# Performance work log

Hardware: AMD Instinct MI355X
Metric: run time of the kernel (lower is better)

Reference implementation:

```python
import jax, jax.numpy as jnp
import numpy as np

F = 128  # num_features
N = 200000

def setup_inputs() -> dict:
    key = jax.random.key(0)
    ks = jax.random.split(key, 9)
    s = 0.05
    inp = {
        "node_feat": jax.random.normal(ks[0], (N, 4 * F), dtype=jnp.float32),
        "U_w": jax.random.normal(ks[1], (F, F), dtype=jnp.float32) * s,
        "U_b": jax.random.normal(ks[2], (F,), dtype=jnp.float32) * s,
        "V_w": jax.random.normal(ks[3], (F, F), dtype=jnp.float32) * s,
        "V_b": jax.random.normal(ks[4], (F,), dtype=jnp.float32) * s,
        "m1_w": jax.random.normal(ks[5], (2 * F, F), dtype=jnp.float32) * s,
        "m1_b": jax.random.normal(ks[6], (F,), dtype=jnp.float32) * s,
        "m2_w": jax.random.normal(ks[7], (F, 3 * F), dtype=jnp.float32) * s,
        "m2_b": jax.random.normal(ks[8], (3 * F,), dtype=jnp.float32) * s,
    }
    return inp

def reference(node_feat, U_w, U_b, V_w, V_b, m1_w, m1_b, m2_w, m2_b):
    node_scalar = node_feat[:, :F]                       # [N, F]
    node_vector = node_feat[:, F:].reshape(-1, 3, F)     # [N, 3, F]
    Uv = jnp.einsum('ncf,fg->ncg', node_vector, U_w) + U_b  # [N, 3, F]
    Vv = jnp.einsum('ncf,fg->ncg', node_vector, V_w) + V_b  # [N, 3, F]
    Vv_norm = jnp.linalg.norm(Vv, axis=1)                # [N, F]
    mlp_in = jnp.concatenate((Vv_norm, node_scalar), axis=1)  # [N, 2F]
    h = jax.nn.silu(mlp_in @ m1_w + m1_b)                # [N, F]
    mlp_out = h @ m2_w + m2_b                            # [N, 3F]
    a_vv, a_sv, a_ss = jnp.split(mlp_out, 3, axis=1)
    delta_v = a_vv[:, None, :] * Uv                      # [N, 3, F]
    inner_prod = jnp.sum(Uv * Vv, axis=1)                # [N, F]
    delta_s = a_sv * inner_prod + a_ss                   # [N, F]
    residual = jnp.concatenate([delta_s, delta_v.reshape(-1, 3 * F)], axis=1)
    return node_feat + residual
```

## Files before the change

kernel.cpp:

```cpp
#include <hip/hip_runtime.h>


#define NT 32
#define STRA 136
#define STRM 264
#define STRH 136

typedef __attribute__((ext_vector_type(8))) short bf16x8;
typedef __attribute__((ext_vector_type(4))) short short4v;
typedef __attribute__((ext_vector_type(4))) float f32x4;

#define MFMA16(a, b, c) __builtin_amdgcn_mfma_f32_16x16x32_bf16(a, b, c, 0, 0, 0)

__device__ __forceinline__ short f2bf(float x) {
    union { float f; unsigned u; } v; v.f = x;
    unsigned r = v.u + 0x7fffu + ((v.u >> 16) & 1u);
    return (short)(r >> 16);
}

__global__ void prep_weights(const float* __restrict__ Uw, const float* __restrict__ Vw,
                             const float* __restrict__ m1w, const float* __restrict__ m2w,
                             short* __restrict__ ws) {
    int idx = blockIdx.x * 256 + threadIdx.x;
    if (idx < 16384) {
        int g = idx >> 7, k = idx & 127;
        ws[idx]         = f2bf(Uw[k * 128 + g]);
        ws[16384 + idx] = f2bf(Vw[k * 128 + g]);
    } else if (idx < 49152) {
        int j = idx - 16384;
        int g = j >> 8, k = j & 255;
        ws[32768 + j] = f2bf(m1w[k * 128 + g]);
    } else if (idx < 98304) {
        int j = idx - 49152;
        int g = j >> 7, k = j & 127;
        ws[65536 + j] = f2bf(m2w[k * 384 + g]);
    }
}

__global__ __launch_bounds__(256, 2)
void painn_fused(const float* __restrict__ nf,
                 const float* __restrict__ Ub, const float* __restrict__ Vb,
                 const float* __restrict__ m1b, const float* __restrict__ m2b,
                 const short* __restrict__ wbuf,
                 float* __restrict__ out) {
    extern __shared__ short lds[];
    short* smA = lds;
    short* smM = smA + 96 * STRA;
    short* smH = smM + 32 * STRM;

    const short* Ut  = wbuf;
    const short* Vt  = wbuf + 16384;
    const short* M1t = wbuf + 32768;
    const short* M2t = wbuf + 65536;

    const int tid  = threadIdx.x;
    const int wave = tid >> 6;
    const int lane = tid & 63;
    const int fc   = lane & 15;
    const int quad = lane >> 4;
    const int ntg0 = wave * 2;
    const long nodebase = (long)blockIdx.x * NT;

    {
        const float* src = nf + nodebase * 512;
        #pragma unroll
        for (int it = 0; it < 16; ++it) {
            int chunk = tid + 256 * it;
            int n = chunk >> 7;
            int col = (chunk & 127) << 2;
            const float4 v = *(const float4*)(src + n * 512 + col);
            short4v s;
            s.x = f2bf(v.x); s.y = f2bf(v.y); s.z = f2bf(v.z); s.w = f2bf(v.w);
            if (col < 128) {
                *(short4v*)&smM[n * STRM + 128 + col] = s;
            } else {
                int vc = col - 128;
                int c = vc >> 7, k = vc & 127;
                *(short4v*)&smA[(c * 32 + n) * STRA + k] = s;
            }
        }
    }
    __syncthreads();

    f32x4 accU[2][3][2], accV[2][3][2];
    #pragma unroll
    for (int nt = 0; nt < 2; ++nt)
        #pragma unroll
        for (int c = 0; c < 3; ++c)
            #pragma unroll
            for (int s = 0; s < 2; ++s) { accU[nt][c][s] = (f32x4)(0.0f); accV[nt][c][s] = (f32x4)(0.0f); }

    #pragma unroll
    for (int kb = 0; kb < 4; ++kb) {
        const int koff = kb * 32 + quad * 8;
        bf16x8 af[3][2];
        #pragma unroll
        for (int c = 0; c < 3; ++c)
            #pragma unroll
            for (int s = 0; s < 2; ++s)
                af[c][s] = *(const bf16x8*)&smA[(c * 32 + s * 16 + fc) * STRA + koff];
        bf16x8 bu[2], bv[2];
        #pragma unroll
        for (int nt = 0; nt < 2; ++nt) {
            const int g = (ntg0 + nt) * 16 + fc;
            bu[nt] = *(const bf16x8*)&Ut[g * 128 + koff];
            bv[nt] = *(const bf16x8*)&Vt[g * 128 + koff];
        }
        #pragma unroll
        for (int nt = 0; nt < 2; ++nt)
            #pragma unroll
            for (int c = 0; c < 3; ++c)
                #pragma unroll
                for (int s = 0; s < 2; ++s) {
                    accU[nt][c][s] = MFMA16(af[c][s], bu[nt], accU[nt][c][s]);
                    accV[nt][c][s] = MFMA16(af[c][s], bv[nt], accV[nt][c][s]);
                }
    }

    float inner[2][2][4];
    #pragma unroll
    for (int nt = 0; nt < 2; ++nt) {
        const int g = (ntg0 + nt) * 16 + fc;
        const float ub = Ub[g], vb = Vb[g];
        #pragma unroll
        for (int s = 0; s < 2; ++s)
            #pragma unroll
            for (int i = 0; i < 4; ++i) {
                float u0 = accU[nt][0][s][i] + ub;
                float u1 = accU[nt][1][s][i] + ub;
                float u2 = accU[nt][2][s][i] + ub;
                float v0 = accV[nt][0][s][i] + vb;
                float v1 = accV[nt][1][s][i] + vb;
                float v2 = accV[nt][2][s][i] + vb;
                accU[nt][0][s][i] = u0; accU[nt][1][s][i] = u1; accU[nt][2][s][i] = u2;
                inner[nt][s][i] = u0 * v0 + u1 * v1 + u2 * v2;
                const float nrm = sqrtf(v0 * v0 + v1 * v1 + v2 * v2);
                const int nl = s * 16 + quad * 4 + i;
                smM[nl * STRM + g] = f2bf(nrm);
            }
    }
    __syncthreads();

    f32x4 acc2[2][2];
    #pragma unroll
    for (int nt = 0; nt < 2; ++nt) { acc2[nt][0] = (f32x4)(0.0f); acc2[nt][1] = (f32x4)(0.0f); }
    #pragma unroll
    for (int kb = 0; kb < 8; ++kb) {
        const int koff = kb * 32 + quad * 8;
        bf16x8 a0 = *(const bf16x8*)&smM[fc * STRM + koff];
        bf16x8 a1 = *(const bf16x8*)&smM[(16 + fc) * STRM + koff];
        #pragma unroll
        for (int nt = 0; nt < 2; ++nt) {
            const int g = (ntg0 + nt) * 16 + fc;
            bf16x8 b = *(const bf16x8*)&M1t[g * 256 + koff];
            acc2[nt][0] = MFMA16(a0, b, acc2[nt][0]);
            acc2[nt][1] = MFMA16(a1, b, acc2[nt][1]);
        }
    }
    #pragma unroll
    for (int nt = 0; nt < 2; ++nt) {
        const int g = (ntg0 + nt) * 16 + fc;
        const float bb = m1b[g];
        #pragma unroll
        for (int mt = 0; mt < 2; ++mt)
            #pragma unroll
            for (int i = 0; i < 4; ++i) {
                const float x = acc2[nt][mt][i] + bb;
                const float sl = x / (1.0f + __expf(-x));
                const int nl = mt * 16 + quad * 4 + i;
                smH[nl * STRH + g] = f2bf(sl);
            }
    }
    __syncthreads();

    f32x4 acc3[3][2][2];
    #pragma unroll
    for (int p = 0; p < 3; ++p)
        #pragma unroll
        for (int nt = 0; nt < 2; ++nt) { acc3[p][nt][0] = (f32x4)(0.0f); acc3[p][nt][1] = (f32x4)(0.0f); }
    #pragma unroll
    for (int kb = 0; kb < 4; ++kb) {
        const int koff = kb * 32 + quad * 8;
        bf16x8 a0 = *(const bf16x8*)&smH[fc * STRH + koff];
        bf16x8 a1 = *(const bf16x8*)&smH[(16 + fc) * STRH + koff];
        #pragma unroll
        for (int p = 0; p < 3; ++p)
            #pragma unroll
            for (int nt = 0; nt < 2; ++nt) {
                const int gcol = p * 128 + (ntg0 + nt) * 16 + fc;
                bf16x8 b = *(const bf16x8*)&M2t[gcol * 128 + koff];
                acc3[p][nt][0] = MFMA16(a0, b, acc3[p][nt][0]);
                acc3[p][nt][1] = MFMA16(a1, b, acc3[p][nt][1]);
            }
    }

    #pragma unroll
    for (int nt = 0; nt < 2; ++nt) {
        const int g = (ntg0 + nt) * 16 + fc;
        const float bvv = m2b[g], bsv = m2b[128 + g], bss = m2b[256 + g];
        #pragma unroll
        for (int mt = 0; mt < 2; ++mt)
            #pragma unroll
            for (int i = 0; i < 4; ++i) {
                const int nl = mt * 16 + quad * 4 + i;
                const long base = (nodebase + nl) * 512;
                const float avv = acc3[0][nt][mt][i] + bvv;
                const float asv = acc3[1][nt][mt][i] + bsv;
                const float ass = acc3[2][nt][mt][i] + bss;
                const float ds  = asv * inner[nt][mt][i] + ass;
                out[base + g] = nf[base + g] + ds;
                #pragma unroll
                for (int c = 0; c < 3; ++c) {
                    const float dv = avv * accU[nt][c][mt][i];
                    out[base + 128 + c * 128 + g] = nf[base + 128 + c * 128 + g] + dv;
                }
            }
    }
}

extern "C" void kernel_launch(void* const* d_in, const int* in_sizes, int n_in,
                              void* d_out, int out_size, void* d_ws, size_t ws_size,
                              hipStream_t stream) {
    (void)in_sizes; (void)n_in; (void)out_size; (void)ws_size;
    const float* node_feat = (const float*)d_in[0];
    const float* U_w  = (const float*)d_in[1];
    const float* U_b  = (const float*)d_in[2];
    const float* V_w  = (const float*)d_in[3];
    const float* V_b  = (const float*)d_in[4];
    const float* m1_w = (const float*)d_in[5];
    const float* m1_b = (const float*)d_in[6];
    const float* m2_w = (const float*)d_in[7];
    const float* m2_b = (const float*)d_in[8];
    short* wbuf = (short*)d_ws;

    prep_weights<<<384, 256, 0, stream>>>(U_w, V_w, m1_w, m2_w, wbuf);

    const int nblocks = 200000 / NT;
    const size_t lds_bytes = (size_t)(96 * STRA + 32 * STRM + 32 * STRH) * sizeof(short);
    painn_fused<<<nblocks, 256, lds_bytes, stream>>>(
        node_feat, U_b, V_b, m1_b, m2_b, wbuf, (float*)d_out);
}
```

Before: 1.107 ms.

## Halve node tile to 16, raise occupancy, batch global loads ahead of use

Cuts the per-block node tile from 32 to 16. This halves accumulator registers and LDS use, and launch bounds now allow 4 blocks per CU instead of 2. The staging loads are issued all at once before the bf16 conversion, and the residual node_feat reads in the epilogue are grouped before the stores so memory latency overlaps. The cost is that each block gets half the reuse of the weight fragments loaded from global/L2, so total weight-fetch traffic doubles.

```diff
diff --git a/kernel.cpp b/kernel.cpp
--- a/kernel.cpp
+++ b/kernel.cpp
@@ -1,9 +1,10 @@
 #include <hip/hip_runtime.h>
 
 
-#define NT 32
+#define NT 16
 #define STRA 136
-#define STRM 264
+#define STRS 136
+#define STRN 136
 #define STRH 136
 
 typedef __attribute__((ext_vector_type(8))) short bf16x8;
@@ -37,7 +38,7 @@
     }
 }
 
-__global__ __launch_bounds__(256, 2)
+__global__ __launch_bounds__(256, 4)
 void painn_fused(const float* __restrict__ nf,
                  const float* __restrict__ Ub, const float* __restrict__ Vb,
                  const float* __restrict__ m1b, const float* __restrict__ m2b,
@@ -45,8 +46,9 @@
                  float* __restrict__ out) {
     extern __shared__ short lds[];
     short* smA = lds;
-    short* smM = smA + 96 * STRA;
-    short* smH = smM + 32 * STRM;
+    short* smS = smA + 48 * STRA;
+    short* smN = smS + 16 * STRS;
+    short* smH = smN + 16 * STRN;
 
     const short* Ut  = wbuf;
     const short* Vt  = wbuf + 16384;
@@ -63,42 +65,46 @@
 
     {
         const float* src = nf + nodebase * 512;
-        #pragma unroll
-        for (int it = 0; it < 16; ++it) {
+        float4 v[8];
+        #pragma unroll
+        for (int it = 0; it < 8; ++it) {
             int chunk = tid + 256 * it;
             int n = chunk >> 7;
             int col = (chunk & 127) << 2;
-            const float4 v = *(const float4*)(src + n * 512 + col);
+            v[it] = *(const float4*)(src + n * 512 + col);
+        }
+        #pragma unroll
+        for (int it = 0; it < 8; ++it) {
+            int chunk = tid + 256 * it;
+            int n = chunk >> 7;
+            int col = (chunk & 127) << 2;
             short4v s;
-            s.x = f2bf(v.x); s.y = f2bf(v.y); s.z = f2bf(v.z); s.w = f2bf(v.w);
+            s.x = f2bf(v[it].x); s.y = f2bf(v[it].y);
+            s.z = f2bf(v[it].z); s.w = f2bf(v[it].w);
             if (col < 128) {
-                *(short4v*)&smM[n * STRM + 128 + col] = s;
+                *(short4v*)&smS[n * STRS + col] = s;
             } else {
                 int vc = col - 128;
                 int c = vc >> 7, k = vc & 127;
-                *(short4v*)&smA[(c * 32 + n) * STRA + k] = s;
+                *(short4v*)&smA[(c * 16 + n) * STRA + k] = s;
             }
         }
     }
     __syncthreads();
 
-    f32x4 accU[2][3][2], accV[2][3][2];
+    f32x4 accU[2][3], accV[2][3];
     #pragma unroll
     for (int nt = 0; nt < 2; ++nt)
         #pragma unroll
-        for (int c = 0; c < 3; ++c)
-            #pragma unroll
-            for (int s = 0; s < 2; ++s) { accU[nt][c][s] = (f32x4)(0.0f); accV[nt][c][s] = (f32x4)(0.0f); }
+        for (int c = 0; c < 3; ++c) { accU[nt][c] = (f32x4)(0.0f); accV[nt][c] = (f32x4)(0.0f); }
 
     #pragma unroll
     for (int kb = 0; kb < 4; ++kb) {
         const int koff = kb * 32 + quad * 8;
-        bf16x8 af[3][2];
+        bf16x8 af[3];
         #pragma unroll
         for (int c = 0; c < 3; ++c)
-            #pragma unroll
-            for (int s = 0; s < 2; ++s)
-                af[c][s] = *(const bf16x8*)&smA[(c * 32 + s * 16 + fc) * STRA + koff];
+            af[c] = *(const bf16x8*)&smA[(c * 16 + fc) * STRA + koff];
         bf16x8 bu[2], bv[2];
         #pragma unroll
         for (int nt = 0; nt < 2; ++nt) {
@@ -109,52 +115,46 @@
         #pragma unroll
         for (int nt = 0; nt < 2; ++nt)
             #pragma unroll
-            for (int c = 0; c < 3; ++c)
-                #pragma unroll
-                for (int s = 0; s < 2; ++s) {
-                    accU[nt][c][s] = MFMA16(af[c][s], bu[nt], accU[nt][c][s]);
-                    accV[nt][c][s] = MFMA16(af[c][s], bv[nt], accV[nt][c][s]);
-                }
-    }
-
-    float inner[2][2][4];
+            for (int c = 0; c < 3; ++c) {
+                accU[nt][c] = MFMA16(af[c], bu[nt], accU[nt][c]);
+                accV[nt][c] = MFMA16(af[c], bv[nt], accV[nt][c]);
+            }
+    }
+
+    float inner[2][4];
     #pragma unroll
     for (int nt = 0; nt < 2; ++nt) {
         const int g = (ntg0 + nt) * 16 + fc;
         const float ub = Ub[g], vb = Vb[g];
         #pragma unroll
-        for (int s = 0; s < 2; ++s)
-            #pragma unroll
-            for (int i = 0; i < 4; ++i) {
-                float u0 = accU[nt][0][s][i] + ub;
-                float u1 = accU[nt][1][s][i] + ub;
-                float u2 = accU[nt][2][s][i] + ub;
-                float v0 = accV[nt][0][s][i] + vb;
-                float v1 = accV[nt][1][s][i] + vb;
-                float v2 = accV[nt][2][s][i] + vb;
-                accU[nt][0][s][i] = u0; accU[nt][1][s][i] = u1; accU[nt][2][s][i] = u2;
-                inner[nt][s][i] = u0 * v0 + u1 * v1 + u2 * v2;
-                const float nrm = sqrtf(v0 * v0 + v1 * v1 + v2 * v2);
-                const int nl = s * 16 + quad * 4 + i;
-                smM[nl * STRM + g] = f2bf(nrm);
-            }
+        for (int i = 0; i < 4; ++i) {
+            float u0 = accU[nt][0][i] + ub;
+            float u1 = accU[nt][1][i] + ub;
+            float u2 = accU[nt][2][i] + ub;
+            float v0 = accV[nt][0][i] + vb;
+            float v1 = accV[nt][1][i] + vb;
+            float v2 = accV[nt][2][i] + vb;
+            accU[nt][0][i] = u0; accU[nt][1][i] = u1; accU[nt][2][i] = u2;
+            inner[nt][i] = u0 * v0 + u1 * v1 + u2 * v2;
+            const float nrm = sqrtf(v0 * v0 + v1 * v1 + v2 * v2);
+            const int nl = quad * 4 + i;
+            smN[nl * STRN + g] = f2bf(nrm);
+        }
     }
     __syncthreads();
 
-    f32x4 acc2[2][2];
-    #pragma unroll
-    for (int nt = 0; nt < 2; ++nt) { acc2[nt][0] = (f32x4)(0.0f); acc2[nt][1] = (f32x4)(0.0f); }
+    f32x4 acc2[2];
+    acc2[0] = (f32x4)(0.0f); acc2[1] = (f32x4)(0.0f);
     #pragma unroll
     for (int kb = 0; kb < 8; ++kb) {
-        const int koff = kb * 32 + quad * 8;
-        bf16x8 a0 = *(const bf16x8*)&smM[fc * STRM + koff];
-        bf16x8 a1 = *(const bf16x8*)&smM[(16 + fc) * STRM + koff];
+        const int kk = (kb & 3) * 32 + quad * 8;
+        bf16x8 a0 = (kb < 4) ? *(const bf16x8*)&smN[fc * STRN + kk]
+                             : *(const bf16x8*)&smS[fc * STRS + kk];
         #pragma unroll
         for (int nt = 0; nt < 2; ++nt) {
             const int g = (ntg0 + nt) * 16 + fc;
-            bf16x8 b = *(const bf16x8*)&M1t[g * 256 + koff];
-            acc2[nt][0] = MFMA16(a0, b, acc2[nt][0]);
-            acc2[nt][1] = MFMA16(a1, b, acc2[nt][1]);
+            bf16x8 b = *(const bf16x8*)&M1t[g * 256 + kb * 32 + quad * 8];
+            acc2[nt] = MFMA16(a0, b, acc2[nt]);
         }
     }
     #pragma unroll
@@ -162,35 +162,29 @@
         const int g = (ntg0 + nt) * 16 + fc;
         const float bb = m1b[g];
         #pragma unroll
-        for (int mt = 0; mt < 2; ++mt)
-            #pragma unroll
-            for (int i = 0; i < 4; ++i) {
-                const float x = acc2[nt][mt][i] + bb;
-                const float sl = x / (1.0f + __expf(-x));
-                const int nl = mt * 16 + quad * 4 + i;
-                smH[nl * STRH + g] = f2bf(sl);
-            }
+        for (int i = 0; i < 4; ++i) {
+            const float x = acc2[nt][i] + bb;
+            const float sl = x / (1.0f + __expf(-x));
+            const int nl = quad * 4 + i;
+            smH[nl * STRH + g] = f2bf(sl);
+        }
     }
     __syncthreads();
 
-    f32x4 acc3[3][2][2];
-    #pragma unroll
-    for (int p = 0; p < 3; ++p)
-        #pragma unroll
-        for (int nt = 0; nt < 2; ++nt) { acc3[p][nt][0] = (f32x4)(0.0f); acc3[p][nt][1] = (f32x4)(0.0f); }
+    f32x4 acc3[3][2];
+    #pragma unroll
+    for (int p = 0; p < 3; ++p) { acc3[p][0] = (f32x4)(0.0f); acc3[p][1] = (f32x4)(0.0f); }
     #pragma unroll
     for (int kb = 0; kb < 4; ++kb) {
         const int koff = kb * 32 + quad * 8;
         bf16x8 a0 = *(const bf16x8*)&smH[fc * STRH + koff];
-        bf16x8 a1 = *(const bf16x8*)&smH[(16 + fc) * STRH + koff];
         #pragma unroll
         for (int p = 0; p < 3; ++p)
             #pragma unroll
             for (int nt = 0; nt < 2; ++nt) {
                 const int gcol = p * 128 + (ntg0 + nt) * 16 + fc;
                 bf16x8 b = *(const bf16x8*)&M2t[gcol * 128 + koff];
-                acc3[p][nt][0] = MFMA16(a0, b, acc3[p][nt][0]);
-                acc3[p][nt][1] = MFMA16(a1, b, acc3[p][nt][1]);
+                acc3[p][nt] = MFMA16(a0, b, acc3[p][nt]);
             }
     }
 
@@ -198,23 +192,27 @@
     for (int nt = 0; nt < 2; ++nt) {
         const int g = (ntg0 + nt) * 16 + fc;
         const float bvv = m2b[g], bsv = m2b[128 + g], bss = m2b[256 + g];
-        #pragma unroll
-        for (int mt = 0; mt < 2; ++mt)
+        float nfv[4][4];
+        #pragma unroll
+        for (int i = 0; i < 4; ++i) {
+            const long base = (nodebase + quad * 4 + i) * 512;
+            nfv[i][0] = nf[base + g];
+            nfv[i][1] = nf[base + 128 + g];
+            nfv[i][2] = nf[base + 256 + g];
+            nfv[i][3] = nf[base + 384 + g];
+        }
+        #pragma unroll
+        for (int i = 0; i < 4; ++i) {
+            const long base = (nodebase + quad * 4 + i) * 512;
+            const float avv = acc3[0][nt][i] + bvv;
+            const float asv = acc3[1][nt][i] + bsv;
+            const float ass = acc3[2][nt][i] + bss;
+            const float ds  = asv * inner[nt][i] + ass;
+            out[base + g] = nfv[i][0] + ds;
             #pragma unroll
-            for (int i = 0; i < 4; ++i) {
-                const int nl = mt * 16 + quad * 4 + i;
-                const long base = (nodebase + nl) * 512;
-                const float avv = acc3[0][nt][mt][i] + bvv;
-                const float asv = acc3[1][nt][mt][i] + bsv;
-                const float ass = acc3[2][nt][mt][i] + bss;
-                const float ds  = asv * inner[nt][mt][i] + ass;
-                out[base + g] = nf[base + g] + ds;
-                #pragma unroll
-                for (int c = 0; c < 3; ++c) {
-                    const float dv = avv * accU[nt][c][mt][i];
-                    out[base + 128 + c * 128 + g] = nf[base + 128 + c * 128 + g] + dv;
-                }
-            }
+            for (int c = 0; c < 3; ++c)
+                out[base + 128 + c * 128 + g] = nfv[i][c + 1] + avv * accU[nt][c][i];
+        }
     }
 }
 
@@ -236,7 +234,7 @@
     prep_weights<<<384, 256, 0, stream>>>(U_w, V_w, m1_w, m2_w, wbuf);
 
     const int nblocks = 200000 / NT;
-    const size_t lds_bytes = (size_t)(96 * STRA + 32 * STRM + 32 * STRH) * sizeof(short);
+    const size_t lds_bytes = (size_t)(48 * STRA + 16 * STRS + 16 * STRN + 16 * STRH) * sizeof(short);
     painn_fused<<<nblocks, 256, lds_bytes, stream>>>(
         node_feat, U_b, V_b, m1_b, m2_b, wbuf, (float*)d_out);
 }
```

New measurement: 936.5 us. -15.4%, faster.
